# Kernel optimization log

Hardware: AMD Instinct MI355X
Metric: run time of the kernel (lower is better)

Reference implementation:

```python
import jax, jax.numpy as jnp
import numpy as np

DATA_DIM = 784
MANIFOLD_DIM = 16
HIDDEN = 256
BATCH = 131072


def setup_inputs() -> dict:
    key = jax.random.key(0)
    ks = jax.random.split(key, 10)
    s = lambda fan_in: 1.0 / np.sqrt(fan_in)
    return {
        "x_t": jax.random.normal(ks[0], (BATCH, DATA_DIM), dtype=jnp.float32),
        "t": jax.random.uniform(ks[1], (BATCH,), dtype=jnp.float32),
        # metric_net: Linear(784,256) -> ReLU -> Linear(256, 16*16)
        "W1": jax.random.uniform(ks[2], (DATA_DIM, HIDDEN), jnp.float32, -s(DATA_DIM), s(DATA_DIM)),
        "b1": jax.random.uniform(ks[3], (HIDDEN,), jnp.float32, -s(DATA_DIM), s(DATA_DIM)),
        "W2": jax.random.uniform(ks[4], (HIDDEN, MANIFOLD_DIM * MANIFOLD_DIM), jnp.float32, -s(HIDDEN), s(HIDDEN)),
        "b2": jax.random.uniform(ks[5], (MANIFOLD_DIM * MANIFOLD_DIM,), jnp.float32, -s(HIDDEN), s(HIDDEN)),
        # project_to_manifold: Linear(784, 16)
        "Wp": jax.random.uniform(ks[6], (DATA_DIM, MANIFOLD_DIM), jnp.float32, -s(DATA_DIM), s(DATA_DIM)),
        "bp": jax.random.uniform(ks[7], (MANIFOLD_DIM,), jnp.float32, -s(DATA_DIM), s(DATA_DIM)),
        # lift_from_manifold: Linear(16, 784)
        "Wl": jax.random.uniform(ks[8], (MANIFOLD_DIM, DATA_DIM), jnp.float32, -s(MANIFOLD_DIM), s(MANIFOLD_DIM)),
        "bl": jax.random.uniform(ks[9], (DATA_DIM,), jnp.float32, -s(MANIFOLD_DIM), s(MANIFOLD_DIM)),
    }


def reference(x_t, t, W1, b1, W2, b2, Wp, bp, Wl, bl):
    d = MANIFOLD_DIM
    # project_to_manifold
    xi = x_t @ Wp + bp  # [B, d]
    # metric_tensor: g = A A^T + 0.1 I, A = metric_net(x).reshape(B, d, d)
    h = jax.nn.relu(x_t @ W1 + b1)
    g_flat = h @ W2 + b2
    A = g_flat.reshape(-1, d, d)
    g = jnp.einsum('bik,bjk->bij', A, A) + 0.1 * jnp.eye(d, dtype=x_t.dtype)
    g_inv = jnp.linalg.inv(g)  # batched small 16x16 inverse
    # latent score: -xi / (t + eps)
    latent_score = -xi / (t[:, None] + 1e-6)
    riemannian_score = jnp.einsum('bij,bj->bi', g_inv, latent_score)
    score_data = riemannian_score @ Wl + bl  # [B, 784]
    return score_data
```

## Files before the change

kernel.cpp:

```cpp
#include <hip/hip_runtime.h>

typedef __attribute__((ext_vector_type(8))) short short8;
typedef __attribute__((ext_vector_type(4))) float f32x4;

#define NT   256
#define ROWS 32

#define W1T_PL  435200
#define W1T_COL 1600
#define W2T_OFF 870400
#define W2T_PL  131072
#define W2T_COL 512
#define WLT_OFF 1132544
#define WLT_PL  25088
#define WLT_COL 32

#define OFF_WCH 0
#define OFF_XT  34816
#define OFF_H   38912
#define OFF_YS  50176
#define OFF_XIP 71680
#define LDS_SZ  79872

#define MFMA16(a,b,c) __builtin_amdgcn_mfma_f32_16x16x32_bf16(a,b,c,0,0,0)

__device__ __forceinline__ unsigned short bf16_rn(float x){
  unsigned u = __float_as_uint(x);
  return (unsigned short)((u + 0x7fffu + ((u >> 16) & 1u)) >> 16);
}
__device__ __forceinline__ float bf16f(unsigned short h){
  return __uint_as_float(((unsigned)h) << 16);
}

__device__ __forceinline__ void glds16(const void* g, void* s){
#if __has_builtin(__builtin_amdgcn_global_load_lds)
  __builtin_amdgcn_global_load_lds((const __attribute__((address_space(1))) void*)g,
                                   (__attribute__((address_space(3))) void*)s, 16, 0, 0);
#else
  const int lane = (int)(threadIdx.x & 63u);
  *(short8*)((char*)s + lane*16) = *(const short8*)((const char*)g);
#endif
}

__global__ __launch_bounds__(256)
void prep_w(const float* __restrict__ W1, const float* __restrict__ W2,
            const float* __restrict__ Wp, const float* __restrict__ Wl,
            unsigned short* __restrict__ ws)
{
  const int u = blockIdx.x * 256 + threadIdx.x;
  float v[8];
  int bh, blo;
  if (u < 27200) {
    int kg = u / 272, col = u - kg*272;
    #pragma unroll
    for (int j = 0; j < 8; ++j) {
      int k = kg*8 + j;
      v[j] = (k < 784) ? ((col < 256) ? W1[k*256 + col] : Wp[k*16 + (col-256)]) : 0.0f;
    }
    bh = col*800 + kg*8; blo = bh + 217600;
  } else if (u < 35392) {
    int q = u - 27200;
    int kg = q >> 8, col = q & 255;
    #pragma unroll
    for (int j = 0; j < 8; ++j) v[j] = W2[(kg*8+j)*256 + col];
    bh = 435200 + col*256 + kg*8; blo = bh + 65536;
  } else if (u < 36960) {
    int q = u - 35392;
    int kg = (q >= 784) ? 1 : 0; int col = q - kg*784;
    #pragma unroll
    for (int j = 0; j < 8; ++j) v[j] = Wl[(kg*8+j)*784 + col];
    bh = 566272 + col*16 + kg*8; blo = bh + 12544;
  } else return;
  short8 hv, lv;
  #pragma unroll
  for (int j = 0; j < 8; ++j) {
    unsigned short hh = bf16_rn(v[j]);
    hv[j] = (short)hh;
    lv[j] = (short)bf16_rn(v[j] - bf16f(hh));
  }
  *(short8*)&ws[bh]  = hv;
  *(short8*)&ws[blo] = lv;
}

__global__ __launch_bounds__(NT, 2)
void riemann_mfma(const float* __restrict__ x, const float* __restrict__ tvec,
                  const float* __restrict__ b1g, const float* __restrict__ b2g,
                  const float* __restrict__ bpg, const float* __restrict__ blg,
                  const char* __restrict__ wst, float* __restrict__ out)
{
  __shared__ __align__(16) char lds[LDS_SZ];
  const int tid = threadIdx.x;
  const int wv  = tid >> 6;
  const int l   = tid & 63;
  const int lr  = l & 15;
  const int lg  = l >> 4;
  const int row0 = (int)blockIdx.x * ROWS;

  const f32x4 Z4 = {0.f, 0.f, 0.f, 0.f};
  const short8 Z8 = {0,0,0,0,0,0,0,0};

  f32x4 acc[2][4];
  f32x4 xia[2];
  #pragma unroll
  for (int mt = 0; mt < 2; ++mt) {
    xia[mt] = Z4;
    #pragma unroll
    for (int nt = 0; nt < 4; ++nt) acc[mt][nt] = Z4;
  }

  const int xrow = tid >> 3;
  const int kq   = tid & 7;
  char* xwrh = lds + OFF_XT + xrow*64 + (((kq>>1) ^ ((xrow>>1)&3))<<4) + (kq&1)*8;

  for (int kc = 0; kc < 25; ++kc) {
    {
      const int kb = kc*32 + kq*4;
      f32x4 xv = Z4;
      if (kb < 784) xv = *(const f32x4*)(x + (long)(row0 + xrow)*784 + kb);
      unsigned long long hq = 0, lq = 0;
      #pragma unroll
      for (int e = 0; e < 4; ++e) {
        unsigned short hh = bf16_rn(xv[e]);
        unsigned short ll = bf16_rn(xv[e] - bf16f(hh));
        hq |= ((unsigned long long)hh) << (16*e);
        lq |= ((unsigned long long)ll) << (16*e);
      }
      *(unsigned long long*)xwrh = hq;
      *(unsigned long long*)(xwrh + 2048) = lq;
    }
    #pragma unroll
    for (int i2 = 0; i2 < 9; ++i2) {
      int i = wv + i2*4;
      if (i < 34) {
        int f = i*64 + l;
        int pl = (f >= 1088) ? 1 : 0;
        int r  = f - pl*1088;
        int col = r >> 2, kgp = r & 3;
        glds16(wst + pl*W1T_PL + col*W1T_COL + kc*64 + ((kgp ^ ((col>>1)&3)) << 4),
               lds + OFF_WCH + i*1024);
      }
    }
    __syncthreads();

    short8 af[2][2];
    #pragma unroll
    for (int mt = 0; mt < 2; ++mt) {
      int row = mt*16 + lr;
      int sl = lg ^ ((row>>1)&3);
      af[0][mt] = *(const short8*)(lds + OFF_XT +        row*64 + sl*16);
      af[1][mt] = *(const short8*)(lds + OFF_XT + 2048 + row*64 + sl*16);
    }
    short8 bfr[2][4];
    #pragma unroll
    for (int nt = 0; nt < 4; ++nt) {
      int col = wv*64 + nt*16 + lr;
      int sl = lg ^ ((col>>1)&3);
      bfr[0][nt] = *(const short8*)(lds + OFF_WCH +         col*64 + sl*16);
      bfr[1][nt] = *(const short8*)(lds + OFF_WCH + 17408 + col*64 + sl*16);
    }
    #pragma unroll
    for (int mt = 0; mt < 2; ++mt)
      #pragma unroll
      for (int nt = 0; nt < 4; ++nt) {
        acc[mt][nt] = MFMA16(af[0][mt], bfr[0][nt], acc[mt][nt]);
        acc[mt][nt] = MFMA16(af[0][mt], bfr[1][nt], acc[mt][nt]);
        acc[mt][nt] = MFMA16(af[1][mt], bfr[0][nt], acc[mt][nt]);
      }
    if ((kc & 3) == wv) {
      int colx = 256 + lr;
      int slx = lg ^ ((colx>>1)&3);
      short8 bx0 = *(const short8*)(lds + OFF_WCH +         colx*64 + slx*16);
      short8 bx1 = *(const short8*)(lds + OFF_WCH + 17408 + colx*64 + slx*16);
      #pragma unroll
      for (int mt = 0; mt < 2; ++mt) {
        xia[mt] = MFMA16(af[0][mt], bx0, xia[mt]);
        xia[mt] = MFMA16(af[0][mt], bx1, xia[mt]);
        xia[mt] = MFMA16(af[1][mt], bx0, xia[mt]);
      }
    }
    __syncthreads();
  }

  #pragma unroll
  for (int nt = 0; nt < 4; ++nt) {
    int col = wv*64 + nt*16 + lr;
    float b1v = b1g[col];
    int cb = (col >> 5)*128 + (col & 7)*4;
    int kgw = (col >> 3) & 3;
    #pragma unroll
    for (int mt = 0; mt < 2; ++mt)
      #pragma unroll
      for (int r = 0; r < 4; ++r) {
        int row = mt*16 + lg*4 + r;
        float v = acc[mt][nt][r] + b1v;
        v = v > 0.f ? v : 0.f;
        *(float*)(lds + OFF_H + row*1024 + cb + ((kgw ^ (row&3))<<5)) = v;
      }
  }
  #pragma unroll
  for (int mt = 0; mt < 2; ++mt)
    #pragma unroll
    for (int r = 0; r < 4; ++r) {
      int row = mt*16 + lg*4 + r;
      *(float*)(lds + OFF_XIP + wv*2048 + row*64 + lr*4) = xia[mt][r];
    }
  __syncthreads();

  f32x4 ac2[2][4];
  #pragma unroll
  for (int mt = 0; mt < 2; ++mt)
    #pragma unroll
    for (int nt = 0; nt < 4; ++nt) ac2[mt][nt] = Z4;

  for (int kc = 0; kc < 8; ++kc) {
    #pragma unroll
    for (int i2 = 0; i2 < 8; ++i2) {
      int i = wv + i2*4;
      int f = i*64 + l;
      int pl = f >> 10;
      int r  = f & 1023;
      int col = r >> 2, kgp = r & 3;
      glds16(wst + W2T_OFF + pl*W2T_PL + col*W2T_COL + kc*64 + ((kgp ^ ((col>>1)&3)) << 4),
             lds + OFF_WCH + i*1024);
    }
    __syncthreads();
    short8 ah[2], alo[2];
    #pragma unroll
    for (int mt = 0; mt < 2; ++mt) {
      int row = mt*16 + lr;
      const char* hb = lds + OFF_H + row*1024 + kc*128 + ((lg ^ (row&3))<<5);
      float hv[8];
      *(f32x4*)&hv[0] = *(const f32x4*)hb;
      *(f32x4*)&hv[4] = *(const f32x4*)(hb + 16);
      #pragma unroll
      for (int j = 0; j < 8; ++j) {
        unsigned short hh = bf16_rn(hv[j]);
        ah[mt][j]  = (short)hh;
        alo[mt][j] = (short)bf16_rn(hv[j] - bf16f(hh));
      }
    }
    short8 b2f[2][4];
    #pragma unroll
    for (int nt = 0; nt < 4; ++nt) {
      int col = wv*64 + nt*16 + lr;
      int sl = lg ^ ((col>>1)&3);
      b2f[0][nt] = *(const short8*)(lds + OFF_WCH +         col*64 + sl*16);
      b2f[1][nt] = *(const short8*)(lds + OFF_WCH + 16384 + col*64 + sl*16);
    }
    #pragma unroll
    for (int mt = 0; mt < 2; ++mt)
      #pragma unroll
      for (int nt = 0; nt < 4; ++nt) {
        ac2[mt][nt] = MFMA16(ah[mt],  b2f[0][nt], ac2[mt][nt]);
        ac2[mt][nt] = MFMA16(ah[mt],  b2f[1][nt], ac2[mt][nt]);
        ac2[mt][nt] = MFMA16(alo[mt], b2f[0][nt], ac2[mt][nt]);
      }
    __syncthreads();
  }
  #pragma unroll
  for (int nt = 0; nt < 4; ++nt) {
    int col = wv*64 + nt*16 + lr;
    float b2v = b2g[col];
    #pragma unroll
    for (int mt = 0; mt < 2; ++mt)
      #pragma unroll
      for (int r = 0; r < 4; ++r) {
        int row = mt*16 + lg*4 + r;
        *(float*)(lds + OFF_WCH + row*1040 + col*4) = ac2[mt][nt][r] + b2v;
      }
  }
  __syncthreads();

  const int grp = tid >> 4;
  const int j16 = tid & 15;
  for (int it = 0; it < 2; ++it) {
    int m = it*16 + grp;
    float a[16];
    const char* gb = lds + OFF_WCH + m*1040 + j16*64;
    *(f32x4*)&a[0]  = *(const f32x4*)(gb);
    *(f32x4*)&a[4]  = *(const f32x4*)(gb + 16);
    *(f32x4*)&a[8]  = *(const f32x4*)(gb + 32);
    *(f32x4*)&a[12] = *(const f32x4*)(gb + 48);
    float xs = *(const float*)(lds + OFF_XIP +        m*64 + j16*4)
             + *(const float*)(lds + OFF_XIP + 2048 + m*64 + j16*4)
             + *(const float*)(lds + OFF_XIP + 4096 + m*64 + j16*4)
             + *(const float*)(lds + OFF_XIP + 6144 + m*64 + j16*4)
             + bpg[j16];
    float rhs = -xs / (tvec[row0 + m] + 1e-6f);
    float rw[16];
    #pragma unroll
    for (int i = 0; i < 16; ++i) {
      float d = (i == j16) ? 0.1f : 0.0f;
      #pragma unroll
      for (int k = 0; k < 16; ++k) d += a[k] * __shfl(a[k], i, 16);
      rw[i] = d;
    }
    float rdv = 0.f;
    #pragma unroll
    for (int k = 0; k < 16; ++k) {
      float piv = __shfl(rw[k], k, 16);
      float rp = 1.0f / piv;
      float f = rw[k] * rp;
      f = (j16 == k) ? 0.0f : f;
      if (j16 == k) rdv = rp;
      #pragma unroll
      for (int q = k+1; q < 16; ++q)
        rw[q] -= f * __shfl(rw[q], k, 16);
      rhs -= f * __shfl(rhs, k, 16);
    }
    float y = rhs * rdv;
    unsigned short yh = bf16_rn(y);
    unsigned short yl = bf16_rn(y - bf16f(yh));
    *(unsigned short*)(lds + OFF_YS +        m*32 + j16*2) = yh;
    *(unsigned short*)(lds + OFF_YS + 1024 + m*32 + j16*2) = yl;
  }
  __syncthreads();

  #pragma unroll
  for (int i2 = 0; i2 < 13; ++i2) {
    int i = wv + i2*4;
    if (i < 49) {
      int f = i*64 + l;
      int pl = (f >= 1568) ? 1 : 0;
      int r  = f - pl*1568;
      int col = r >> 1, kg = r & 1;
      glds16(wst + WLT_OFF + pl*WLT_PL + col*WLT_COL + kg*16,
             lds + OFF_WCH + i*1024);
    }
  }
  __syncthreads();

  short8 ya[2][2];
  #pragma unroll
  for (int p = 0; p < 2; ++p)
    #pragma unroll
    for (int mt = 0; mt < 2; ++mt) {
      short8 v = Z8;
      if (lg < 2) v = *(const short8*)(lds + OFF_YS + p*1024 + (mt*16 + lr)*32 + lg*16);
      ya[p][mt] = v;
    }

  for (int nt = wv; nt < 49; nt += 4) {
    short8 w0 = Z8, w1v = Z8;
    if (lg < 2) {
      int col = nt*16 + lr;
      w0  = *(const short8*)(lds + OFF_WCH +         col*32 + lg*16);
      w1v = *(const short8*)(lds + OFF_WCH + 25088 + col*32 + lg*16);
    }
    float blv = blg[nt*16 + lr];
    #pragma unroll
    for (int mt = 0; mt < 2; ++mt) {
      f32x4 a5 = Z4;
      a5 = MFMA16(ya[0][mt], w0,  a5);
      a5 = MFMA16(ya[0][mt], w1v, a5);
      a5 = MFMA16(ya[1][mt], w0,  a5);
      #pragma unroll
      for (int r = 0; r < 4; ++r)
        out[(long)(row0 + mt*16 + lg*4 + r)*784 + nt*16 + lr] = a5[r] + blv;
    }
  }
}

extern "C" void kernel_launch(void* const* d_in, const int* in_sizes, int n_in,
                              void* d_out, int out_size, void* d_ws, size_t ws_size,
                              hipStream_t stream)
{
  (void)n_in; (void)out_size; (void)ws_size;
  const float* x  = (const float*)d_in[0];
  const float* t  = (const float*)d_in[1];
  const float* W1 = (const float*)d_in[2];
  const float* b1 = (const float*)d_in[3];
  const float* W2 = (const float*)d_in[4];
  const float* b2 = (const float*)d_in[5];
  const float* Wp = (const float*)d_in[6];
  const float* bp = (const float*)d_in[7];
  const float* Wl = (const float*)d_in[8];
  const float* bl = (const float*)d_in[9];
  float* out = (float*)d_out;
  const int B = in_sizes[1];

  hipLaunchKernelGGL(prep_w, dim3(145), dim3(256), 0, stream,
                     W1, W2, Wp, Wl, (unsigned short*)d_ws);
  hipLaunchKernelGGL(riemann_mfma, dim3(B / ROWS), dim3(NT), 0, stream,
                     x, t, b1, b2, bp, bl, (const char*)d_ws, out);
}
```

Baseline: 1.184 ms.

## Double-buffer W1/x staging and prefetch W2, Wl tiles during compute

The first GEMM loop now double-buffers the W1 tiles and the bf16 split of x in LDS, and register-prefetches x two steps ahead, so global loads overlap the MFMAs and one barrier per iteration is dropped. The ReLU hidden activations are split into bf16 hi/lo once, at the point they are written, instead of being converted inside every step of the second GEMM. W2 chunks are prefetched after a barrier within each iteration, and the Wl load is issued before the 16x16 solves so it overlaps them. The LDS layout is reshuffled to reuse regions, which adds risk of aliasing hazards, and the added register pressure may lower occupancy.

```diff
diff --git a/kernel.cpp b/kernel.cpp
--- a/kernel.cpp
+++ b/kernel.cpp
@@ -15,12 +15,14 @@
 #define WLT_PL  25088
 #define WLT_COL 32
 
-#define OFF_WCH 0
-#define OFF_XT  34816
-#define OFF_H   38912
-#define OFF_YS  50176
-#define OFF_XIP 71680
-#define LDS_SZ  79872
+#define OFF_W0   0
+#define OFF_W1   34816
+#define OFF_H    34816
+#define OFF_X0   69632
+#define OFF_X1   73728
+#define OFF_XIP  69632
+#define OFF_YS   77824
+#define LDS_SZ   79872
 
 #define MFMA16(a,b,c) __builtin_amdgcn_mfma_f32_16x16x32_bf16(a,b,c,0,0,0)
 
@@ -110,24 +112,30 @@
 
   const int xrow = tid >> 3;
   const int kq   = tid & 7;
-  char* xwrh = lds + OFF_XT + xrow*64 + (((kq>>1) ^ ((xrow>>1)&3))<<4) + (kq&1)*8;
-
-  for (int kc = 0; kc < 25; ++kc) {
-    {
-      const int kb = kc*32 + kq*4;
-      f32x4 xv = Z4;
-      if (kb < 784) xv = *(const f32x4*)(x + (long)(row0 + xrow)*784 + kb);
-      unsigned long long hq = 0, lq = 0;
-      #pragma unroll
-      for (int e = 0; e < 4; ++e) {
-        unsigned short hh = bf16_rn(xv[e]);
-        unsigned short ll = bf16_rn(xv[e] - bf16f(hh));
-        hq |= ((unsigned long long)hh) << (16*e);
-        lq |= ((unsigned long long)ll) << (16*e);
-      }
-      *(unsigned long long*)xwrh = hq;
-      *(unsigned long long*)(xwrh + 2048) = lq;
-    }
+  const int xwoff = xrow*64 + (((kq>>1) ^ ((xrow>>1)&3))<<4) + (kq&1)*8;
+
+  auto loadX = [&](int ct)->f32x4 {
+    f32x4 v = Z4;
+    if (ct < 25) {
+      int kb = ct*32 + kq*4;
+      if (kb < 784) v = *(const f32x4*)(x + (long)(row0 + xrow)*784 + kb);
+    }
+    return v;
+  };
+  auto writeX = [&](const f32x4& xv, int slot){
+    unsigned long long hq = 0, lq = 0;
+    #pragma unroll
+    for (int e = 0; e < 4; ++e) {
+      unsigned short hh = bf16_rn(xv[e]);
+      unsigned short ll = bf16_rn(xv[e] - bf16f(hh));
+      hq |= ((unsigned long long)hh) << (16*e);
+      lq |= ((unsigned long long)ll) << (16*e);
+    }
+    char* b = lds + (slot ? OFF_X1 : OFF_X0) + xwoff;
+    *(unsigned long long*)b = hq;
+    *(unsigned long long*)(b + 2048) = lq;
+  };
+  auto stageW1 = [&](int t, int slot){
     #pragma unroll
     for (int i2 = 0; i2 < 9; ++i2) {
       int i = wv + i2*4;
@@ -136,27 +144,43 @@
         int pl = (f >= 1088) ? 1 : 0;
         int r  = f - pl*1088;
         int col = r >> 2, kgp = r & 3;
-        glds16(wst + pl*W1T_PL + col*W1T_COL + kc*64 + ((kgp ^ ((col>>1)&3)) << 4),
-               lds + OFF_WCH + i*1024);
-      }
-    }
-    __syncthreads();
+        glds16(wst + pl*W1T_PL + col*W1T_COL + t*64 + ((kgp ^ ((col>>1)&3)) << 4),
+               lds + (slot ? OFF_W1 : OFF_W0) + i*1024);
+      }
+    }
+  };
+
+  f32x4 xv0 = loadX(0);
+  stageW1(0, 0);
+  writeX(xv0, 0);
+  f32x4 xv = loadX(1);
+  __syncthreads();
+
+  for (int t = 0; t < 25; ++t) {
+    const int cur = t & 1, nxt = cur ^ 1;
+    if (t < 24) {
+      stageW1(t + 1, nxt);
+      writeX(xv, nxt);
+      xv = loadX(t + 2);
+    }
+    const char* Xb = lds + (cur ? OFF_X1 : OFF_X0);
+    const char* Wb = lds + (cur ? OFF_W1 : OFF_W0);
 
     short8 af[2][2];
     #pragma unroll
     for (int mt = 0; mt < 2; ++mt) {
       int row = mt*16 + lr;
       int sl = lg ^ ((row>>1)&3);
-      af[0][mt] = *(const short8*)(lds + OFF_XT +        row*64 + sl*16);
-      af[1][mt] = *(const short8*)(lds + OFF_XT + 2048 + row*64 + sl*16);
+      af[0][mt] = *(const short8*)(Xb +        row*64 + sl*16);
+      af[1][mt] = *(const short8*)(Xb + 2048 + row*64 + sl*16);
     }
     short8 bfr[2][4];
     #pragma unroll
     for (int nt = 0; nt < 4; ++nt) {
       int col = wv*64 + nt*16 + lr;
       int sl = lg ^ ((col>>1)&3);
-      bfr[0][nt] = *(const short8*)(lds + OFF_WCH +         col*64 + sl*16);
-      bfr[1][nt] = *(const short8*)(lds + OFF_WCH + 17408 + col*64 + sl*16);
+      bfr[0][nt] = *(const short8*)(Wb +         col*64 + sl*16);
+      bfr[1][nt] = *(const short8*)(Wb + 17408 + col*64 + sl*16);
     }
     #pragma unroll
     for (int mt = 0; mt < 2; ++mt)
@@ -166,11 +190,11 @@
         acc[mt][nt] = MFMA16(af[0][mt], bfr[1][nt], acc[mt][nt]);
         acc[mt][nt] = MFMA16(af[1][mt], bfr[0][nt], acc[mt][nt]);
       }
-    if ((kc & 3) == wv) {
+    if ((t & 3) == wv) {
       int colx = 256 + lr;
       int slx = lg ^ ((colx>>1)&3);
-      short8 bx0 = *(const short8*)(lds + OFF_WCH +         colx*64 + slx*16);
-      short8 bx1 = *(const short8*)(lds + OFF_WCH + 17408 + colx*64 + slx*16);
+      short8 bx0 = *(const short8*)(Wb +         colx*64 + slx*16);
+      short8 bx1 = *(const short8*)(Wb + 17408 + colx*64 + slx*16);
       #pragma unroll
       for (int mt = 0; mt < 2; ++mt) {
         xia[mt] = MFMA16(af[0][mt], bx0, xia[mt]);
@@ -181,12 +205,21 @@
     __syncthreads();
   }
 
+  {
+    #pragma unroll
+    for (int i2 = 0; i2 < 8; ++i2) {
+      int i = wv + i2*4;
+      int f = i*64 + l;
+      int pl = f >> 10, r = f & 1023;
+      int col = r >> 2, kgp = r & 3;
+      glds16(wst + W2T_OFF + pl*W2T_PL + col*W2T_COL + 0*64 + ((kgp ^ ((col>>1)&3)) << 4),
+             lds + OFF_W0 + i*1024);
+    }
+  }
   #pragma unroll
   for (int nt = 0; nt < 4; ++nt) {
     int col = wv*64 + nt*16 + lr;
     float b1v = b1g[col];
-    int cb = (col >> 5)*128 + (col & 7)*4;
-    int kgw = (col >> 3) & 3;
     #pragma unroll
     for (int mt = 0; mt < 2; ++mt)
       #pragma unroll
@@ -194,7 +227,11 @@
         int row = mt*16 + lg*4 + r;
         float v = acc[mt][nt][r] + b1v;
         v = v > 0.f ? v : 0.f;
-        *(float*)(lds + OFF_H + row*1024 + cb + ((kgw ^ (row&3))<<5)) = v;
+        unsigned short hh = bf16_rn(v);
+        unsigned short ll = bf16_rn(v - bf16f(hh));
+        int bo = (row*512 + col*2) ^ ((row&7)<<4);
+        *(unsigned short*)(lds + OFF_H +         bo) = hh;
+        *(unsigned short*)(lds + OFF_H + 16384 + bo) = ll;
       }
   }
   #pragma unroll
@@ -212,40 +249,34 @@
     #pragma unroll
     for (int nt = 0; nt < 4; ++nt) ac2[mt][nt] = Z4;
 
-  for (int kc = 0; kc < 8; ++kc) {
-    #pragma unroll
-    for (int i2 = 0; i2 < 8; ++i2) {
-      int i = wv + i2*4;
-      int f = i*64 + l;
-      int pl = f >> 10;
-      int r  = f & 1023;
-      int col = r >> 2, kgp = r & 3;
-      glds16(wst + W2T_OFF + pl*W2T_PL + col*W2T_COL + kc*64 + ((kgp ^ ((col>>1)&3)) << 4),
-             lds + OFF_WCH + i*1024);
-    }
-    __syncthreads();
+  for (int t = 0; t < 8; ++t) {
     short8 ah[2], alo[2];
     #pragma unroll
     for (int mt = 0; mt < 2; ++mt) {
       int row = mt*16 + lr;
-      const char* hb = lds + OFF_H + row*1024 + kc*128 + ((lg ^ (row&3))<<5);
-      float hv[8];
-      *(f32x4*)&hv[0] = *(const f32x4*)hb;
-      *(f32x4*)&hv[4] = *(const f32x4*)(hb + 16);
-      #pragma unroll
-      for (int j = 0; j < 8; ++j) {
-        unsigned short hh = bf16_rn(hv[j]);
-        ah[mt][j]  = (short)hh;
-        alo[mt][j] = (short)bf16_rn(hv[j] - bf16f(hh));
-      }
+      int bo = (row*512 + t*64 + lg*16) ^ ((row&7)<<4);
+      ah[mt]  = *(const short8*)(lds + OFF_H +         bo);
+      alo[mt] = *(const short8*)(lds + OFF_H + 16384 + bo);
     }
     short8 b2f[2][4];
     #pragma unroll
     for (int nt = 0; nt < 4; ++nt) {
       int col = wv*64 + nt*16 + lr;
       int sl = lg ^ ((col>>1)&3);
-      b2f[0][nt] = *(const short8*)(lds + OFF_WCH +         col*64 + sl*16);
-      b2f[1][nt] = *(const short8*)(lds + OFF_WCH + 16384 + col*64 + sl*16);
+      b2f[0][nt] = *(const short8*)(lds + OFF_W0 +         col*64 + sl*16);
+      b2f[1][nt] = *(const short8*)(lds + OFF_W0 + 16384 + col*64 + sl*16);
+    }
+    __syncthreads();
+    if (t < 7) {
+      #pragma unroll
+      for (int i2 = 0; i2 < 8; ++i2) {
+        int i = wv + i2*4;
+        int f = i*64 + l;
+        int pl = f >> 10, r = f & 1023;
+        int col = r >> 2, kgp = r & 3;
+        glds16(wst + W2T_OFF + pl*W2T_PL + col*W2T_COL + (t+1)*64 + ((kgp ^ ((col>>1)&3)) << 4),
+               lds + OFF_W0 + i*1024);
+      }
     }
     #pragma unroll
     for (int mt = 0; mt < 2; ++mt)
@@ -266,33 +297,60 @@
       #pragma unroll
       for (int r = 0; r < 4; ++r) {
         int row = mt*16 + lg*4 + r;
-        *(float*)(lds + OFF_WCH + row*1040 + col*4) = ac2[mt][nt][r] + b2v;
+        *(float*)(lds + OFF_W0 + row*1024 + col*4) = ac2[mt][nt][r] + b2v;
       }
   }
   __syncthreads();
 
   const int grp = tid >> 4;
   const int j16 = tid & 15;
-  for (int it = 0; it < 2; ++it) {
-    int m = it*16 + grp;
-    float a[16];
-    const char* gb = lds + OFF_WCH + m*1040 + j16*64;
-    *(f32x4*)&a[0]  = *(const f32x4*)(gb);
-    *(f32x4*)&a[4]  = *(const f32x4*)(gb + 16);
-    *(f32x4*)&a[8]  = *(const f32x4*)(gb + 32);
-    *(f32x4*)&a[12] = *(const f32x4*)(gb + 48);
-    float xs = *(const float*)(lds + OFF_XIP +        m*64 + j16*4)
-             + *(const float*)(lds + OFF_XIP + 2048 + m*64 + j16*4)
-             + *(const float*)(lds + OFF_XIP + 4096 + m*64 + j16*4)
-             + *(const float*)(lds + OFF_XIP + 6144 + m*64 + j16*4)
-             + bpg[j16];
-    float rhs = -xs / (tvec[row0 + m] + 1e-6f);
+  float aA[16], aB[16];
+  {
+    const char* g0 = lds + OFF_W0 + grp*1024 + j16*64;
+    const char* g1 = lds + OFF_W0 + (16+grp)*1024 + j16*64;
+    *(f32x4*)&aA[0]  = *(const f32x4*)(g0);
+    *(f32x4*)&aA[4]  = *(const f32x4*)(g0 + 16);
+    *(f32x4*)&aA[8]  = *(const f32x4*)(g0 + 32);
+    *(f32x4*)&aA[12] = *(const f32x4*)(g0 + 48);
+    *(f32x4*)&aB[0]  = *(const f32x4*)(g1);
+    *(f32x4*)&aB[4]  = *(const f32x4*)(g1 + 16);
+    *(f32x4*)&aB[8]  = *(const f32x4*)(g1 + 32);
+    *(f32x4*)&aB[12] = *(const f32x4*)(g1 + 48);
+  }
+  float bpv = bpg[j16];
+  float xs0 = *(const float*)(lds + OFF_XIP +        grp*64 + j16*4)
+            + *(const float*)(lds + OFF_XIP + 2048 + grp*64 + j16*4)
+            + *(const float*)(lds + OFF_XIP + 4096 + grp*64 + j16*4)
+            + *(const float*)(lds + OFF_XIP + 6144 + grp*64 + j16*4) + bpv;
+  float xs1 = *(const float*)(lds + OFF_XIP +        (16+grp)*64 + j16*4)
+            + *(const float*)(lds + OFF_XIP + 2048 + (16+grp)*64 + j16*4)
+            + *(const float*)(lds + OFF_XIP + 4096 + (16+grp)*64 + j16*4)
+            + *(const float*)(lds + OFF_XIP + 6144 + (16+grp)*64 + j16*4) + bpv;
+  float rhs0 = -xs0 / (tvec[row0 + grp] + 1e-6f);
+  float rhs1 = -xs1 / (tvec[row0 + 16 + grp] + 1e-6f);
+  __syncthreads();
+
+  {
+    #pragma unroll
+    for (int i2 = 0; i2 < 13; ++i2) {
+      int i = wv + i2*4;
+      if (i < 49) {
+        int f = i*64 + l;
+        int pl = (f >= 1568) ? 1 : 0;
+        int r  = f - pl*1568;
+        int col = r >> 1, kg = r & 1;
+        glds16(wst + WLT_OFF + pl*WLT_PL + col*WLT_COL + kg*16,
+               lds + OFF_W0 + i*1024);
+      }
+    }
+  }
+  {
     float rw[16];
     #pragma unroll
     for (int i = 0; i < 16; ++i) {
       float d = (i == j16) ? 0.1f : 0.0f;
       #pragma unroll
-      for (int k = 0; k < 16; ++k) d += a[k] * __shfl(a[k], i, 16);
+      for (int k = 0; k < 16; ++k) d += aA[k] * __shfl(aA[k], i, 16);
       rw[i] = d;
     }
     float rdv = 0.f;
@@ -306,27 +364,41 @@
       #pragma unroll
       for (int q = k+1; q < 16; ++q)
         rw[q] -= f * __shfl(rw[q], k, 16);
-      rhs -= f * __shfl(rhs, k, 16);
-    }
-    float y = rhs * rdv;
+      rhs0 -= f * __shfl(rhs0, k, 16);
+    }
+    float y = rhs0 * rdv;
     unsigned short yh = bf16_rn(y);
     unsigned short yl = bf16_rn(y - bf16f(yh));
-    *(unsigned short*)(lds + OFF_YS +        m*32 + j16*2) = yh;
-    *(unsigned short*)(lds + OFF_YS + 1024 + m*32 + j16*2) = yl;
-  }
-  __syncthreads();
-
-  #pragma unroll
-  for (int i2 = 0; i2 < 13; ++i2) {
-    int i = wv + i2*4;
-    if (i < 49) {
-      int f = i*64 + l;
-      int pl = (f >= 1568) ? 1 : 0;
-      int r  = f - pl*1568;
-      int col = r >> 1, kg = r & 1;
-      glds16(wst + WLT_OFF + pl*WLT_PL + col*WLT_COL + kg*16,
-             lds + OFF_WCH + i*1024);
-    }
+    *(unsigned short*)(lds + OFF_YS +        grp*32 + j16*2) = yh;
+    *(unsigned short*)(lds + OFF_YS + 1024 + grp*32 + j16*2) = yl;
+  }
+  {
+    float rw[16];
+    #pragma unroll
+    for (int i = 0; i < 16; ++i) {
+      float d = (i == j16) ? 0.1f : 0.0f;
+      #pragma unroll
+      for (int k = 0; k < 16; ++k) d += aB[k] * __shfl(aB[k], i, 16);
+      rw[i] = d;
+    }
+    float rdv = 0.f;
+    #pragma unroll
+    for (int k = 0; k < 16; ++k) {
+      float piv = __shfl(rw[k], k, 16);
+      float rp = 1.0f / piv;
+      float f = rw[k] * rp;
+      f = (j16 == k) ? 0.0f : f;
+      if (j16 == k) rdv = rp;
+      #pragma unroll
+      for (int q = k+1; q < 16; ++q)
+        rw[q] -= f * __shfl(rw[q], k, 16);
+      rhs1 -= f * __shfl(rhs1, k, 16);
+    }
+    float y = rhs1 * rdv;
+    unsigned short yh = bf16_rn(y);
+    unsigned short yl = bf16_rn(y - bf16f(yh));
+    *(unsigned short*)(lds + OFF_YS +        (16+grp)*32 + j16*2) = yh;
+    *(unsigned short*)(lds + OFF_YS + 1024 + (16+grp)*32 + j16*2) = yl;
   }
   __syncthreads();
 
@@ -344,8 +416,8 @@
     short8 w0 = Z8, w1v = Z8;
     if (lg < 2) {
       int col = nt*16 + lr;
-      w0  = *(const short8*)(lds + OFF_WCH +         col*32 + lg*16);
-      w1v = *(const short8*)(lds + OFF_WCH + 25088 + col*32 + lg*16);
+      w0  = *(const short8*)(lds + OFF_W0 +         col*32 + lg*16);
+      w1v = *(const short8*)(lds + OFF_W0 + 25088 + col*32 + lg*16);
     }
     float blv = blg[nt*16 + lr];
     #pragma unroll
```

After: 1.089 ms. -8.0%, faster.
